# Performance work log

Measured on AMD Instinct MI355X. Metric: run time of the kernel, lower is better.

Reference implementation:

```python
import jax, jax.numpy as jnp
import numpy as np

L, B, T, D, H = 8, 4, 1024, 1024, 16
DH = D // H
TPB, NB = 16, 64  # tokens_per_block, max_blocks; T == TPB*NB
EPS = 1e-5


def _block_causal_mask():
    idx = jnp.arange(T)
    causal = idx[:, None] >= idx[None, :]
    blk = idx // TPB
    block_diag = blk[:, None] == blk[None, :]
    return causal | block_diag  # [T, T] bool


def _ln(x, g, b):
    mu = jnp.mean(x, axis=-1, keepdims=True)
    var = jnp.mean(jnp.square(x - mu), axis=-1, keepdims=True)
    return (x - mu) * jax.lax.rsqrt(var + EPS) * g + b


def setup_inputs() -> dict:
    key = jax.random.key(0)
    ks = jax.random.split(key, 8)
    s = 0.02
    inp = {
        'sequences': jax.random.normal(ks[0], (B, T, D), jnp.float32),
        'Wq': jax.random.normal(ks[1], (L, D, D), jnp.float32) * s,
        'bq': jnp.zeros((L, D), jnp.float32),
        'Wk': jax.random.normal(ks[2], (L, D, D), jnp.float32) * s,
        'bk': jnp.zeros((L, D), jnp.float32),
        'Wv': jax.random.normal(ks[3], (L, D, D), jnp.float32) * s,
        'bv': jnp.zeros((L, D), jnp.float32),
        'Wp': jax.random.normal(ks[4], (L, D, D), jnp.float32) * s,
        'bp': jnp.zeros((L, D), jnp.float32),
        'ln1_g': jnp.ones((L, D), jnp.float32),
        'ln1_b': jnp.zeros((L, D), jnp.float32),
        'ln2_g': jnp.ones((L, D), jnp.float32),
        'ln2_b': jnp.zeros((L, D), jnp.float32),
        'W1': jax.random.normal(ks[5], (L, D, 4 * D), jnp.float32) * s,
        'b1': jnp.zeros((L, 4 * D), jnp.float32),
        'W2': jax.random.normal(ks[6], (L, 4 * D, D), jnp.float32) * s,
        'b2': jnp.zeros((L, D), jnp.float32),
        'lnf_g': jnp.ones((D,), jnp.float32),
        'lnf_b': jnp.zeros((D,), jnp.float32),
    }
    return inp


def reference(sequences, Wq, bq, Wk, bk, Wv, bv, Wp, bp,
              ln1_g, ln1_b, ln2_g, ln2_b, W1, b1, W2, b2, lnf_g, lnf_b):
    mask = _block_causal_mask()
    scale = 1.0 / np.sqrt(DH)
    x = sequences
    for i in range(L):
        h = _ln(x, ln1_g[i], ln1_b[i])
        q = (h @ Wq[i] + bq[i]).reshape(B, T, H, DH)
        k = (h @ Wk[i] + bk[i]).reshape(B, T, H, DH)
        v = (h @ Wv[i] + bv[i]).reshape(B, T, H, DH)
        att = jnp.einsum('bthd,bshd->bhts', q, k) * scale  # [B,H,T,T]
        att = jnp.where(mask, att, -jnp.inf)
        att = jax.nn.softmax(att, axis=-1)
        y = jnp.einsum('bhts,bshd->bthd', att, v).reshape(B, T, D)
        x = x + (y @ Wp[i] + bp[i])
        h2 = _ln(x, ln2_g[i], ln2_b[i])
        ff = jax.nn.gelu(h2 @ W1[i] + b1[i], approximate=False) @ W2[i] + b2[i]
        x = x + ff
    return _ln(x, lnf_g, lnf_b)
```

## Files before the change

### kernel.cpp

```cpp
#include <hip/hip_runtime.h>
#include <hip/hip_bf16.h>
#include <math.h>

#define B_ 4
#define T_ 1024
#define D_ 1024
#define H_ 16
#define DH_ 64
#define M_ 4096
#define QSTR_ 3072
#define EPS_ 1e-5f

typedef __attribute__((ext_vector_type(4))) float f32x4;
typedef __attribute__((ext_vector_type(8))) short s16x8;

#if __has_builtin(__builtin_amdgcn_exp2f)
#define EXP2F __builtin_amdgcn_exp2f
#else
#define EXP2F exp2f
#endif

__device__ __forceinline__ float gelu_f(float x) {
  return 0.5f * x * (1.0f + erff(x * 0.70710678118654752f));
}
__device__ __forceinline__ float b2f(unsigned short u) {
  union { unsigned int i; float f; } c; c.i = ((unsigned int)u) << 16; return c.f;
}
__device__ __forceinline__ unsigned short f2b(float f) {
  __hip_bfloat16 h = __float2bfloat16(f);
  return *reinterpret_cast<unsigned short*>(&h);
}
__device__ __forceinline__ void g2l16(void* l, const void* g) {
  __builtin_amdgcn_global_load_lds(
      (const __attribute__((address_space(1))) void*)g,
      (__attribute__((address_space(3))) void*)l, 16, 0, 0);
}

template<bool BF16OUT>
__global__ __launch_bounds__(256) void ln_kernel(
    const float* __restrict__ in, void* __restrict__ out,
    const float* __restrict__ g, const float* __restrict__ b) {
  const int row = blockIdx.x;
  const int tid = threadIdx.x;
  const float* rp = in + (size_t)row * D_;
  float4 v = *reinterpret_cast<const float4*>(rp + tid * 4);
  float s = v.x + v.y + v.z + v.w;
  float s2 = v.x * v.x + v.y * v.y + v.z * v.z + v.w * v.w;
#pragma unroll
  for (int off = 1; off < 64; off <<= 1) {
    s += __shfl_xor(s, off);
    s2 += __shfl_xor(s2, off);
  }
  __shared__ float red[2][4];
  const int wid = tid >> 6;
  if ((tid & 63) == 0) { red[0][wid] = s; red[1][wid] = s2; }
  __syncthreads();
  s = red[0][0] + red[0][1] + red[0][2] + red[0][3];
  s2 = red[1][0] + red[1][1] + red[1][2] + red[1][3];
  const float mu = s * (1.0f / D_);
  const float var = s2 * (1.0f / D_) - mu * mu;
  const float rs = rsqrtf(var + EPS_);
  float4 gv = *reinterpret_cast<const float4*>(g + tid * 4);
  float4 bv = *reinterpret_cast<const float4*>(b + tid * 4);
  float o0 = (v.x - mu) * rs * gv.x + bv.x;
  float o1 = (v.y - mu) * rs * gv.y + bv.y;
  float o2 = (v.z - mu) * rs * gv.z + bv.z;
  float o3 = (v.w - mu) * rs * gv.w + bv.w;
  if (BF16OUT) {
    ushort4 pk;
    pk.x = f2b(o0); pk.y = f2b(o1); pk.z = f2b(o2); pk.w = f2b(o3);
    *reinterpret_cast<ushort4*>((unsigned short*)out + (size_t)row * D_ + tid * 4) = pk;
  } else {
    *reinterpret_cast<float4*>((float*)out + (size_t)row * D_ + tid * 4) =
        make_float4(o0, o1, o2, o3);
  }
}

__global__ __launch_bounds__(256) void concat_bias(
    const float* __restrict__ bq, const float* __restrict__ bk,
    const float* __restrict__ bv, float* __restrict__ out) {
  const int i = blockIdx.x * 256 + threadIdx.x;
  const int l = i / QSTR_, c = i % QSTR_;
  const float* src = (c < 1024) ? bq : ((c < 2048) ? bk : bv);
  out[i] = src[l * 1024 + (c & 1023)];
}

__device__ __forceinline__ void transpose_tile(
    const float* __restrict__ src, int sld,
    __hip_bfloat16* __restrict__ dst, int dld, int k0, int n0) {
  __shared__ float tile[32][33];
  const int t = threadIdx.x;
  const int r = t >> 3;
  const int cq = (t & 7) * 4;
  float4 vv = *reinterpret_cast<const float4*>(src + (size_t)(k0 + r) * sld + n0 + cq);
  tile[r][cq + 0] = vv.x; tile[r][cq + 1] = vv.y;
  tile[r][cq + 2] = vv.z; tile[r][cq + 3] = vv.w;
  __syncthreads();
  ushort4 o;
  o.x = f2b(tile[cq + 0][r]); o.y = f2b(tile[cq + 1][r]);
  o.z = f2b(tile[cq + 2][r]); o.w = f2b(tile[cq + 3][r]);
  *reinterpret_cast<ushort4*>((unsigned short*)dst + (size_t)(n0 + r) * dld + k0 + cq) = o;
}

struct TPack { const float* s[4]; __hip_bfloat16* d[4]; };

__global__ __launch_bounds__(256) void transpose4(TPack p) {
  transpose_tile(p.s[blockIdx.z], 1024, p.d[blockIdx.z], 1024,
                 blockIdx.x * 32, blockIdx.y * 32);
}
__global__ __launch_bounds__(256) void transpose1(
    const float* __restrict__ src, int sld,
    __hip_bfloat16* __restrict__ dst, int dld) {
  transpose_tile(src, sld, dst, dld, blockIdx.x * 32, blockIdx.y * 32);
}

template<int MODE, int BN>
__global__ __launch_bounds__(256) void gemm_mfma(
    const __hip_bfloat16* __restrict__ A,
    const __hip_bfloat16* __restrict__ Bt,
    const float* __restrict__ bias,
    void* __restrict__ Cout, int N, int K) {
  __shared__ short As[2][128 * 32];
  __shared__ short Bs[2][BN * 32];
  int bid = blockIdx.y * gridDim.x + blockIdx.x;
  const int nwg = gridDim.x * gridDim.y;
  bid = (bid & 7) * (nwg >> 3) + (bid >> 3);
  const int gn = (bid % gridDim.x) * BN;
  const int gm = (bid / gridDim.x) * 128;

  const int tid = threadIdx.x;
  const int wid = tid >> 6, lane = tid & 63;
  constexpr int MR = (BN == 128) ? 4 : 2;
  const int wm = (BN == 128) ? (wid >> 1) : wid;
  const int wn = (BN == 128) ? (wid & 1) : 0;
  const int fr = lane & 15, kg = lane >> 4;

  const int ldr = lane >> 2;
  const int ldk = (lane & 3) * 8;
  const unsigned short* ap =
      (const unsigned short*)A + (size_t)(gm + wid * 32 + ldr) * K + ldk;
  const unsigned short* bp =
      (const unsigned short*)Bt +
      (size_t)(gn + ((BN == 128) ? wid * 32 : wid * 16) + ldr) * K + ldk;

  {
    g2l16((char*)As[0] + (wid * 2) * 1024, ap);
    g2l16((char*)As[0] + (wid * 2 + 1) * 1024, ap + (size_t)16 * K);
    if (BN == 128) {
      g2l16((char*)Bs[0] + (wid * 2) * 1024, bp);
      g2l16((char*)Bs[0] + (wid * 2 + 1) * 1024, bp + (size_t)16 * K);
    } else {
      g2l16((char*)Bs[0] + wid * 1024, bp);
    }
    ap += 32; bp += 32;
  }
  asm volatile("s_waitcnt vmcnt(0)" ::: "memory");
  __syncthreads();

  f32x4 acc[MR][4] = {};
  int cur = 0;
  for (int kt = 0; kt < K; kt += 32) {
    if (kt + 32 < K) {
      g2l16((char*)As[cur ^ 1] + (wid * 2) * 1024, ap);
      g2l16((char*)As[cur ^ 1] + (wid * 2 + 1) * 1024, ap + (size_t)16 * K);
      if (BN == 128) {
        g2l16((char*)Bs[cur ^ 1] + (wid * 2) * 1024, bp);
        g2l16((char*)Bs[cur ^ 1] + (wid * 2 + 1) * 1024, bp + (size_t)16 * K);
      } else {
        g2l16((char*)Bs[cur ^ 1] + wid * 1024, bp);
      }
      ap += 32; bp += 32;
    }
    s16x8 af[MR], bfr[4];
#pragma unroll
    for (int m = 0; m < MR; ++m)
      af[m] = *reinterpret_cast<const s16x8*>(
          &As[cur][(wm * (16 * MR) + m * 16 + fr) * 32 + kg * 8]);
#pragma unroll
    for (int n = 0; n < 4; ++n)
      bfr[n] = *reinterpret_cast<const s16x8*>(
          &Bs[cur][(wn * 64 + n * 16 + fr) * 32 + kg * 8]);
#pragma unroll
    for (int m = 0; m < MR; ++m)
#pragma unroll
      for (int n = 0; n < 4; ++n)
        acc[m][n] = __builtin_amdgcn_mfma_f32_16x16x32_bf16(af[m], bfr[n], acc[m][n], 0, 0, 0);
    asm volatile("s_waitcnt vmcnt(0)" ::: "memory");
    __syncthreads();
    cur ^= 1;
  }

  const int r0 = gm + wm * (16 * MR);
  const int c0 = gn + wn * 64;
  float bb[4];
#pragma unroll
  for (int n = 0; n < 4; ++n)
    bb[n] = bias ? bias[c0 + n * 16 + fr] : 0.0f;
#pragma unroll
  for (int m = 0; m < MR; ++m) {
#pragma unroll
    for (int j = 0; j < 4; ++j) {
      const int row = r0 + m * 16 + kg * 4 + j;
#pragma unroll
      for (int n = 0; n < 4; ++n) {
        float val = acc[m][n][j] + bb[n];
        const size_t idx = (size_t)row * N + c0 + n * 16 + fr;
        if (MODE == 0) {
          ((unsigned short*)Cout)[idx] = f2b(val);
        } else if (MODE == 1) {
          float* cp = (float*)Cout + idx;
          *cp = *cp + val;
        } else {
          ((unsigned short*)Cout)[idx] = f2b(gelu_f(val));
        }
      }
    }
  }
}

__global__ __launch_bounds__(256) void attn_mfma(
    const __hip_bfloat16* __restrict__ qkv, __hip_bfloat16* __restrict__ yg) {
  const int qb = 15 - blockIdx.x;
  const int hh = blockIdx.y;
  const int bb = blockIdx.z;
  __shared__ short Ks[64 * 64];
  __shared__ short Vt[64 * 64];
  __shared__ short Ps[64 * 64];
  const int tid = threadIdx.x;
  const int wid = tid >> 6, lane = tid & 63;
  const int fr = lane & 15, kgv = lane >> 4;
  const size_t qb_base = (size_t)bb * T_ * QSTR_ + (size_t)hh * DH_;
  const unsigned short* qgp = (const unsigned short*)qkv + qb_base;
  const unsigned short* kgp = (const unsigned short*)qkv + qb_base + 1024;
  const unsigned short* vgp = (const unsigned short*)qkv + qb_base + 2048;
  const float C = 0.125f * 1.4426950408889634f;

  {
    const int r8 = lane >> 3, cp = lane & 7;
#pragma unroll
    for (int u = 0; u < 2; ++u) {
      const int row = wid * 16 + u * 8 + r8;
      const int c16 = cp ^ (row & 7);
      g2l16((char*)Ps + (wid * 16 + u * 8) * 128,
            qgp + (size_t)(qb * 64 + row) * QSTR_ + c16 * 8);
    }
  }
  asm volatile("s_waitcnt vmcnt(0)" ::: "memory");
  __syncthreads();
  s16x8 qf[2];
  {
    const int row = wid * 16 + fr;
    const char* rp = (const char*)Ps + row * 128;
    qf[0] = *reinterpret_cast<const s16x8*>(rp + (((0 + kgv) ^ (row & 7)) << 4));
    qf[1] = *reinterpret_cast<const s16x8*>(rp + (((4 + kgv) ^ (row & 7)) << 4));
  }

  f32x4 acco[4] = {};
  float m_run[4] = {-INFINITY, -INFINITY, -INFINITY, -INFINITY};
  float l_run[4] = {};

  for (int kb = 0; kb <= qb; ++kb) {
    __syncthreads();
    {
      const int r8 = lane >> 3, cp = lane & 7;
#pragma unroll
      for (int u = 0; u < 2; ++u) {
        const int row = wid * 16 + u * 8 + r8;
        const int c16 = cp ^ (row & 7);
        g2l16((char*)Ks + (wid * 16 + u * 8) * 128,
              kgp + (size_t)(kb * 64 + row) * QSTR_ + c16 * 8);
      }
    }
    {
      const int kv0 = tid >> 3;
      const int d0 = (tid & 7) * 8;
      const int rot = tid & 7;
#pragma unroll
      for (int u = 0; u < 2; ++u) {
        const int kv = u * 32 + kv0;
        s16x8 sv = *reinterpret_cast<const s16x8*>(
            vgp + (size_t)(kb * 64 + kv) * QSTR_ + d0);
#pragma unroll
        for (int j = 0; j < 8; ++j) {
          const int jj = (j + rot) & 7;
          const int d = d0 + jj;
          *(short*)((char*)Vt + d * 128 + ((((kv >> 3) ^ jj) & 7) << 4) + (kv & 7) * 2) = sv[jj];
        }
      }
    }
    asm volatile("s_waitcnt vmcnt(0)" ::: "memory");
    __syncthreads();

    f32x4 accs[4] = {};
#pragma unroll
    for (int n = 0; n < 4; ++n) {
      const int row = n * 16 + fr;
      const char* rp = (const char*)Ks + row * 128;
      s16x8 kf0 = *reinterpret_cast<const s16x8*>(rp + (((0 + kgv) ^ (row & 7)) << 4));
      s16x8 kf1 = *reinterpret_cast<const s16x8*>(rp + (((4 + kgv) ^ (row & 7)) << 4));
      accs[n] = __builtin_amdgcn_mfma_f32_16x16x32_bf16(qf[0], kf0, accs[n], 0, 0, 0);
      accs[n] = __builtin_amdgcn_mfma_f32_16x16x32_bf16(qf[1], kf1, accs[n], 0, 0, 0);
    }

    const bool diag = (kb == qb);
    float mloc[4];
#pragma unroll
    for (int j = 0; j < 4; ++j) {
      float mm = -3.0e38f;
#pragma unroll
      for (int n = 0; n < 4; ++n)
        if (!(diag && n > wid)) mm = fmaxf(mm, accs[n][j]);
      mloc[j] = mm;
    }
#pragma unroll
    for (int off = 1; off < 16; off <<= 1)
#pragma unroll
      for (int j = 0; j < 4; ++j) mloc[j] = fmaxf(mloc[j], __shfl_xor(mloc[j], off));
    float aj[4];
#pragma unroll
    for (int j = 0; j < 4; ++j) {
      const float mn = fmaxf(m_run[j], mloc[j]);
      aj[j] = EXP2F((m_run[j] - mn) * C);
      m_run[j] = mn;
    }
    float psum[4] = {};
    unsigned short pb[4][4];
#pragma unroll
    for (int n = 0; n < 4; ++n) {
      const bool dead = diag && (n > wid);
#pragma unroll
      for (int j = 0; j < 4; ++j) {
        float p = dead ? 0.0f : EXP2F((accs[n][j] - m_run[j]) * C);
        psum[j] += p;
        pb[n][j] = f2b(p);
      }
    }
#pragma unroll
    for (int j = 0; j < 4; ++j) l_run[j] = l_run[j] * aj[j] + psum[j];
#pragma unroll
    for (int dt = 0; dt < 4; ++dt)
#pragma unroll
      for (int j = 0; j < 4; ++j) acco[dt][j] *= aj[j];
#pragma unroll
    for (int n = 0; n < 4; ++n) {
      const int c16b = n * 2 + (fr >> 3);
#pragma unroll
      for (int j = 0; j < 4; ++j) {
        const int row = wid * 16 + kgv * 4 + j;
        *(short*)((char*)Ps + row * 128 + (((c16b ^ (row & 7)) & 7) << 4) + (fr & 7) * 2) =
            (short)pb[n][j];
      }
    }
#pragma unroll
    for (int kk = 0; kk < 2; ++kk) {
      const int prow = wid * 16 + fr;
      s16x8 pf = *reinterpret_cast<const s16x8*>(
          (const char*)Ps + prow * 128 + ((((kk * 4 + kgv) ^ (prow & 7)) & 7) << 4));
#pragma unroll
      for (int dt = 0; dt < 4; ++dt) {
        const int vrow = dt * 16 + fr;
        s16x8 vf = *reinterpret_cast<const s16x8*>(
            (const char*)Vt + vrow * 128 + ((((kk * 4 + kgv) ^ (vrow & 7)) & 7) << 4));
        acco[dt] = __builtin_amdgcn_mfma_f32_16x16x32_bf16(pf, vf, acco[dt], 0, 0, 0);
      }
    }
  }

#pragma unroll
  for (int off = 1; off < 16; off <<= 1)
#pragma unroll
    for (int j = 0; j < 4; ++j) l_run[j] += __shfl_xor(l_run[j], off);
  float inv[4];
#pragma unroll
  for (int j = 0; j < 4; ++j) inv[j] = 1.0f / l_run[j];
  unsigned short* yp = (unsigned short*)yg + (size_t)bb * T_ * D_ + (size_t)hh * DH_;
#pragma unroll
  for (int dt = 0; dt < 4; ++dt)
#pragma unroll
    for (int j = 0; j < 4; ++j) {
      const int row = qb * 64 + wid * 16 + kgv * 4 + j;
      yp[(size_t)row * D_ + dt * 16 + fr] = f2b(acco[dt][j] * inv[j]);
    }
}

extern "C" void kernel_launch(void* const* d_in, const int* in_sizes, int n_in,
                              void* d_out, int out_size, void* d_ws, size_t ws_size,
                              hipStream_t stream) {
  (void)in_sizes; (void)n_in; (void)out_size; (void)ws_size;
  const float* seq  = (const float*)d_in[0];
  const float* Wq   = (const float*)d_in[1];
  const float* bq   = (const float*)d_in[2];
  const float* Wk   = (const float*)d_in[3];
  const float* bk   = (const float*)d_in[4];
  const float* Wv   = (const float*)d_in[5];
  const float* bv   = (const float*)d_in[6];
  const float* Wp   = (const float*)d_in[7];
  const float* bp   = (const float*)d_in[8];
  const float* ln1g = (const float*)d_in[9];
  const float* ln1b = (const float*)d_in[10];
  const float* ln2g = (const float*)d_in[11];
  const float* ln2b = (const float*)d_in[12];
  const float* W1   = (const float*)d_in[13];
  const float* b1   = (const float*)d_in[14];
  const float* W2   = (const float*)d_in[15];
  const float* b2   = (const float*)d_in[16];
  const float* lnfg = (const float*)d_in[17];
  const float* lnfb = (const float*)d_in[18];

  float* x = (float*)d_out;
  char* ws = (char*)d_ws;
  const size_t MB = 1024ull * 1024ull;
  typedef __hip_bfloat16 bf16;
  bf16*  wtqkv = (bf16*)(ws + 0 * MB);
  bf16*  wtp   = (bf16*)(ws + 6 * MB);
  bf16*  wtF1  = (bf16*)(ws + 8 * MB);
  bf16*  wtF2  = (bf16*)(ws + 16 * MB);
  bf16*  hb    = (bf16*)(ws + 24 * MB);
  bf16*  qkv   = (bf16*)(ws + 32 * MB);
  bf16*  mid   = (bf16*)(ws + 56 * MB);
  float* bqkv  = (float*)(ws + 88 * MB);

  hipMemcpyAsync(x, seq, (size_t)M_ * D_ * sizeof(float), hipMemcpyDeviceToDevice, stream);

  const dim3 blk(256);
  concat_bias<<<96, blk, 0, stream>>>(bq, bk, bv, bqkv);

  for (int i = 0; i < 8; ++i) {
    const size_t wo  = (size_t)i * D_ * D_;
    const size_t vo  = (size_t)i * D_;
    const size_t w1o = (size_t)i * D_ * 4 * D_;

    ln_kernel<true><<<M_, blk, 0, stream>>>(x, hb, ln1g + vo, ln1b + vo);
    TPack tp;
    tp.s[0] = Wq + wo; tp.s[1] = Wk + wo; tp.s[2] = Wv + wo; tp.s[3] = Wp + wo;
    tp.d[0] = wtqkv; tp.d[1] = wtqkv + 1024 * 1024; tp.d[2] = wtqkv + 2048 * 1024;
    tp.d[3] = wtp;
    transpose4<<<dim3(32, 32, 4), blk, 0, stream>>>(tp);
    gemm_mfma<0, 128><<<dim3(24, 32), blk, 0, stream>>>(
        hb, wtqkv, bqkv + (size_t)i * QSTR_, qkv, QSTR_, 1024);
    attn_mfma<<<dim3(16, 16, 4), blk, 0, stream>>>(qkv, hb);
    gemm_mfma<1, 64><<<dim3(16, 32), blk, 0, stream>>>(hb, wtp, bp + vo, x, 1024, 1024);
    ln_kernel<true><<<M_, blk, 0, stream>>>(x, hb, ln2g + vo, ln2b + vo);
    transpose1<<<dim3(32, 128), blk, 0, stream>>>(W1 + w1o, 4096, wtF1, 1024);
    gemm_mfma<2, 128><<<dim3(32, 32), blk, 0, stream>>>(
        hb, wtF1, b1 + (size_t)i * 4096, mid, 4096, 1024);
    transpose1<<<dim3(128, 32), blk, 0, stream>>>(W2 + w1o, 1024, wtF2, 4096);
    gemm_mfma<1, 64><<<dim3(16, 32), blk, 0, stream>>>(
        mid, wtF2, b2 + vo, x, 1024, 4096);
  }
  ln_kernel<false><<<M_, blk, 0, stream>>>(x, x, lnfg, lnfb);
}
```

Measured before the change: 2.441 ms.

## Process 128 query rows per attention block and fuse all weight transposes

```diff
diff --git a/kernel.cpp b/kernel.cpp
--- a/kernel.cpp
+++ b/kernel.cpp
@@ -102,16 +102,32 @@
   *reinterpret_cast<ushort4*>((unsigned short*)dst + (size_t)(n0 + r) * dld + k0 + cq) = o;
 }
 
-struct TPack { const float* s[4]; __hip_bfloat16* d[4]; };
-
-__global__ __launch_bounds__(256) void transpose4(TPack p) {
-  transpose_tile(p.s[blockIdx.z], 1024, p.d[blockIdx.z], 1024,
-                 blockIdx.x * 32, blockIdx.y * 32);
-}
-__global__ __launch_bounds__(256) void transpose1(
-    const float* __restrict__ src, int sld,
-    __hip_bfloat16* __restrict__ dst, int dld) {
-  transpose_tile(src, sld, dst, dld, blockIdx.x * 32, blockIdx.y * 32);
+struct TrAll {
+  const float *wq, *wk, *wv, *wp, *w1, *w2;
+  __hip_bfloat16 *dqkv, *dp, *d1, *d2;
+};
+
+__global__ __launch_bounds__(256) void transpose_all(TrAll a) {
+  const int t = blockIdx.x;
+  const float* src;
+  __hip_bfloat16* dst;
+  int sld, dld, k0, n0;
+  if (t < 4096) {
+    const int m = t >> 10, tile = t & 1023;
+    k0 = (tile >> 5) * 32; n0 = (tile & 31) * 32;
+    src = (m == 0) ? a.wq : (m == 1) ? a.wk : (m == 2) ? a.wv : a.wp;
+    sld = 1024; dld = 1024;
+    dst = (m < 3) ? (a.dqkv + (size_t)m * 1024 * 1024) : a.dp;
+  } else if (t < 8192) {
+    const int tile = t - 4096;
+    k0 = (tile & 31) * 32; n0 = (tile >> 5) * 32;
+    src = a.w1; sld = 4096; dst = a.d1; dld = 1024;
+  } else {
+    const int tile = t - 8192;
+    k0 = (tile >> 5) * 32; n0 = (tile & 31) * 32;
+    src = a.w2; sld = 1024; dst = a.d2; dld = 4096;
+  }
+  transpose_tile(src, sld, dst, dld, k0, n0);
 }
 
 template<int MODE, int BN>
@@ -220,46 +236,52 @@
 
 __global__ __launch_bounds__(256) void attn_mfma(
     const __hip_bfloat16* __restrict__ qkv, __hip_bfloat16* __restrict__ yg) {
-  const int qb = 15 - blockIdx.x;
+  const int qb = 7 - blockIdx.x;
   const int hh = blockIdx.y;
   const int bb = blockIdx.z;
+  __shared__ short Qs[128 * 64];
   __shared__ short Ks[64 * 64];
   __shared__ short Vt[64 * 64];
-  __shared__ short Ps[64 * 64];
   const int tid = threadIdx.x;
   const int wid = tid >> 6, lane = tid & 63;
-  const int fr = lane & 15, kgv = lane >> 4;
+  const int fr = lane & 15, kg = lane >> 4;
   const size_t qb_base = (size_t)bb * T_ * QSTR_ + (size_t)hh * DH_;
   const unsigned short* qgp = (const unsigned short*)qkv + qb_base;
-  const unsigned short* kgp = (const unsigned short*)qkv + qb_base + 1024;
-  const unsigned short* vgp = (const unsigned short*)qkv + qb_base + 2048;
+  const unsigned short* kgp = qgp + 1024;
+  const unsigned short* vgp = qgp + 2048;
   const float C = 0.125f * 1.4426950408889634f;
 
   {
     const int r8 = lane >> 3, cp = lane & 7;
 #pragma unroll
-    for (int u = 0; u < 2; ++u) {
-      const int row = wid * 16 + u * 8 + r8;
+    for (int u = 0; u < 4; ++u) {
+      const int row = wid * 32 + u * 8 + r8;
       const int c16 = cp ^ (row & 7);
-      g2l16((char*)Ps + (wid * 16 + u * 8) * 128,
-            qgp + (size_t)(qb * 64 + row) * QSTR_ + c16 * 8);
+      g2l16((char*)Qs + (wid * 32 + u * 8) * 128,
+            qgp + (size_t)(qb * 128 + row) * QSTR_ + c16 * 8);
     }
   }
   asm volatile("s_waitcnt vmcnt(0)" ::: "memory");
   __syncthreads();
-  s16x8 qf[2];
-  {
-    const int row = wid * 16 + fr;
-    const char* rp = (const char*)Ps + row * 128;
-    qf[0] = *reinterpret_cast<const s16x8*>(rp + (((0 + kgv) ^ (row & 7)) << 4));
-    qf[1] = *reinterpret_cast<const s16x8*>(rp + (((4 + kgv) ^ (row & 7)) << 4));
-  }
-
-  f32x4 acco[4] = {};
-  float m_run[4] = {-INFINITY, -INFINITY, -INFINITY, -INFINITY};
-  float l_run[4] = {};
-
-  for (int kb = 0; kb <= qb; ++kb) {
+  s16x8 qf[2][2];
+#pragma unroll
+  for (int rg = 0; rg < 2; ++rg) {
+    const int row = wid * 32 + rg * 16 + fr;
+    const char* rp = (const char*)Qs + row * 128;
+    qf[rg][0] = *reinterpret_cast<const s16x8*>(rp + (((0 + kg) ^ (row & 7)) << 4));
+    qf[rg][1] = *reinterpret_cast<const s16x8*>(rp + (((4 + kg) ^ (row & 7)) << 4));
+  }
+
+  f32x4 acco[2][4] = {};
+  float m_run[2][4], l_run[2][4];
+#pragma unroll
+  for (int rg = 0; rg < 2; ++rg)
+#pragma unroll
+    for (int j = 0; j < 4; ++j) { m_run[rg][j] = -INFINITY; l_run[rg][j] = 0.f; }
+
+  const int q16hi = qb * 8 + wid * 2 + 1;
+  const int ntile = 2 * qb + 2;
+  for (int kt = 0; kt < ntile; ++kt) {
     __syncthreads();
     {
       const int r8 = lane >> 3, cp = lane & 7;
@@ -268,7 +290,7 @@
         const int row = wid * 16 + u * 8 + r8;
         const int c16 = cp ^ (row & 7);
         g2l16((char*)Ks + (wid * 16 + u * 8) * 128,
-              kgp + (size_t)(kb * 64 + row) * QSTR_ + c16 * 8);
+              kgp + (size_t)(kt * 64 + row) * QSTR_ + c16 * 8);
       }
     }
     {
@@ -279,7 +301,7 @@
       for (int u = 0; u < 2; ++u) {
         const int kv = u * 32 + kv0;
         s16x8 sv = *reinterpret_cast<const s16x8*>(
-            vgp + (size_t)(kb * 64 + kv) * QSTR_ + d0);
+            vgp + (size_t)(kt * 64 + kv) * QSTR_ + d0);
 #pragma unroll
         for (int j = 0; j < 8; ++j) {
           const int jj = (j + rot) & 7;
@@ -291,96 +313,101 @@
     asm volatile("s_waitcnt vmcnt(0)" ::: "memory");
     __syncthreads();
 
-    f32x4 accs[4] = {};
-#pragma unroll
-    for (int n = 0; n < 4; ++n) {
-      const int row = n * 16 + fr;
-      const char* rp = (const char*)Ks + row * 128;
-      s16x8 kf0 = *reinterpret_cast<const s16x8*>(rp + (((0 + kgv) ^ (row & 7)) << 4));
-      s16x8 kf1 = *reinterpret_cast<const s16x8*>(rp + (((4 + kgv) ^ (row & 7)) << 4));
-      accs[n] = __builtin_amdgcn_mfma_f32_16x16x32_bf16(qf[0], kf0, accs[n], 0, 0, 0);
-      accs[n] = __builtin_amdgcn_mfma_f32_16x16x32_bf16(qf[1], kf1, accs[n], 0, 0, 0);
-    }
-
-    const bool diag = (kb == qb);
-    float mloc[4];
-#pragma unroll
-    for (int j = 0; j < 4; ++j) {
-      float mm = -3.0e38f;
-#pragma unroll
-      for (int n = 0; n < 4; ++n)
-        if (!(diag && n > wid)) mm = fmaxf(mm, accs[n][j]);
-      mloc[j] = mm;
-    }
-#pragma unroll
-    for (int off = 1; off < 16; off <<= 1)
-#pragma unroll
-      for (int j = 0; j < 4; ++j) mloc[j] = fmaxf(mloc[j], __shfl_xor(mloc[j], off));
-    float aj[4];
-#pragma unroll
-    for (int j = 0; j < 4; ++j) {
-      const float mn = fmaxf(m_run[j], mloc[j]);
-      aj[j] = EXP2F((m_run[j] - mn) * C);
-      m_run[j] = mn;
-    }
-    float psum[4] = {};
-    unsigned short pb[4][4];
-#pragma unroll
-    for (int n = 0; n < 4; ++n) {
-      const bool dead = diag && (n > wid);
+    if (kt * 4 <= q16hi) {
+      f32x4 accs[2][4] = {};
+#pragma unroll
+      for (int n = 0; n < 4; ++n) {
+        const int row = n * 16 + fr;
+        const char* rp = (const char*)Ks + row * 128;
+        s16x8 kf0 = *reinterpret_cast<const s16x8*>(rp + (((0 + kg) ^ (row & 7)) << 4));
+        s16x8 kf1 = *reinterpret_cast<const s16x8*>(rp + (((4 + kg) ^ (row & 7)) << 4));
+#pragma unroll
+        for (int rg = 0; rg < 2; ++rg) {
+          accs[rg][n] = __builtin_amdgcn_mfma_f32_16x16x32_bf16(qf[rg][0], kf0, accs[rg][n], 0, 0, 0);
+          accs[rg][n] = __builtin_amdgcn_mfma_f32_16x16x32_bf16(qf[rg][1], kf1, accs[rg][n], 0, 0, 0);
+        }
+      }
+#pragma unroll
+      for (int rg = 0; rg < 2; ++rg) {
+        const int q16 = qb * 8 + wid * 2 + rg;
+        float mloc[4] = {-3.0e38f, -3.0e38f, -3.0e38f, -3.0e38f};
+#pragma unroll
+        for (int n = 0; n < 4; ++n)
+          if (kt * 4 + n <= q16)
+#pragma unroll
+            for (int j = 0; j < 4; ++j) mloc[j] = fmaxf(mloc[j], accs[rg][n][j]);
+#pragma unroll
+        for (int off = 1; off < 16; off <<= 1)
+#pragma unroll
+          for (int j = 0; j < 4; ++j) mloc[j] = fmaxf(mloc[j], __shfl_xor(mloc[j], off));
+        float a_[4];
+#pragma unroll
+        for (int j = 0; j < 4; ++j) {
+          const float mn = fmaxf(m_run[rg][j], mloc[j]);
+          a_[j] = EXP2F((m_run[rg][j] - mn) * C);
+          m_run[rg][j] = mn;
+        }
+        float psum[4] = {};
+#pragma unroll
+        for (int n = 0; n < 4; ++n) {
+          const bool dead = (kt * 4 + n > q16);
+          const int c16b = n * 2 + (fr >> 3);
+#pragma unroll
+          for (int j = 0; j < 4; ++j) {
+            float p = dead ? 0.0f : EXP2F((accs[rg][n][j] - m_run[rg][j]) * C);
+            psum[j] += p;
+            const int row = wid * 32 + rg * 16 + kg * 4 + j;
+            *(short*)((char*)Qs + row * 128 + (((c16b ^ (row & 7)) & 7) << 4) + (fr & 7) * 2) =
+                (short)f2b(p);
+          }
+        }
+#pragma unroll
+        for (int j = 0; j < 4; ++j) l_run[rg][j] = l_run[rg][j] * a_[j] + psum[j];
+#pragma unroll
+        for (int dt = 0; dt < 4; ++dt)
+#pragma unroll
+          for (int j = 0; j < 4; ++j) acco[rg][dt][j] *= a_[j];
+      }
+#pragma unroll
+      for (int rg = 0; rg < 2; ++rg) {
+        const int prow = wid * 32 + rg * 16 + fr;
+        const char* pp = (const char*)Qs + prow * 128;
+#pragma unroll
+        for (int kk = 0; kk < 2; ++kk) {
+          const s16x8 pf = *reinterpret_cast<const s16x8*>(
+              pp + ((((kk * 4 + kg) ^ (prow & 7)) & 7) << 4));
+#pragma unroll
+          for (int dt = 0; dt < 4; ++dt) {
+            const int vrow = dt * 16 + fr;
+            const s16x8 vf = *reinterpret_cast<const s16x8*>(
+                (const char*)Vt + vrow * 128 + ((((kk * 4 + kg) ^ (vrow & 7)) & 7) << 4));
+            acco[rg][dt] = __builtin_amdgcn_mfma_f32_16x16x32_bf16(pf, vf, acco[rg][dt], 0, 0, 0);
+          }
+        }
+      }
+    }
+  }
+
+#pragma unroll
+  for (int off = 1; off < 16; off <<= 1)
+#pragma unroll
+    for (int rg = 0; rg < 2; ++rg)
+#pragma unroll
+      for (int j = 0; j < 4; ++j) l_run[rg][j] += __shfl_xor(l_run[rg][j], off);
+  unsigned short* yp = (unsigned short*)yg + (size_t)bb * T_ * D_ + (size_t)hh * DH_;
+#pragma unroll
+  for (int rg = 0; rg < 2; ++rg) {
+    float inv[4];
+#pragma unroll
+    for (int j = 0; j < 4; ++j) inv[j] = 1.0f / l_run[rg][j];
+#pragma unroll
+    for (int dt = 0; dt < 4; ++dt)
 #pragma unroll
       for (int j = 0; j < 4; ++j) {
-        float p = dead ? 0.0f : EXP2F((accs[n][j] - m_run[j]) * C);
-        psum[j] += p;
-        pb[n][j] = f2b(p);
-      }
-    }
-#pragma unroll
-    for (int j = 0; j < 4; ++j) l_run[j] = l_run[j] * aj[j] + psum[j];
-#pragma unroll
-    for (int dt = 0; dt < 4; ++dt)
-#pragma unroll
-      for (int j = 0; j < 4; ++j) acco[dt][j] *= aj[j];
-#pragma unroll
-    for (int n = 0; n < 4; ++n) {
-      const int c16b = n * 2 + (fr >> 3);
-#pragma unroll
-      for (int j = 0; j < 4; ++j) {
-        const int row = wid * 16 + kgv * 4 + j;
-        *(short*)((char*)Ps + row * 128 + (((c16b ^ (row & 7)) & 7) << 4) + (fr & 7) * 2) =
-            (short)pb[n][j];
-      }
-    }
-#pragma unroll
-    for (int kk = 0; kk < 2; ++kk) {
-      const int prow = wid * 16 + fr;
-      s16x8 pf = *reinterpret_cast<const s16x8*>(
-          (const char*)Ps + prow * 128 + ((((kk * 4 + kgv) ^ (prow & 7)) & 7) << 4));
-#pragma unroll
-      for (int dt = 0; dt < 4; ++dt) {
-        const int vrow = dt * 16 + fr;
-        s16x8 vf = *reinterpret_cast<const s16x8*>(
-            (const char*)Vt + vrow * 128 + ((((kk * 4 + kgv) ^ (vrow & 7)) & 7) << 4));
-        acco[dt] = __builtin_amdgcn_mfma_f32_16x16x32_bf16(pf, vf, acco[dt], 0, 0, 0);
-      }
-    }
-  }
-
-#pragma unroll
-  for (int off = 1; off < 16; off <<= 1)
-#pragma unroll
-    for (int j = 0; j < 4; ++j) l_run[j] += __shfl_xor(l_run[j], off);
-  float inv[4];
-#pragma unroll
-  for (int j = 0; j < 4; ++j) inv[j] = 1.0f / l_run[j];
-  unsigned short* yp = (unsigned short*)yg + (size_t)bb * T_ * D_ + (size_t)hh * DH_;
-#pragma unroll
-  for (int dt = 0; dt < 4; ++dt)
-#pragma unroll
-    for (int j = 0; j < 4; ++j) {
-      const int row = qb * 64 + wid * 16 + kgv * 4 + j;
-      yp[(size_t)row * D_ + dt * 16 + fr] = f2b(acco[dt][j] * inv[j]);
-    }
+        const int row = qb * 128 + wid * 32 + rg * 16 + kg * 4 + j;
+        yp[(size_t)row * D_ + dt * 16 + fr] = f2b(acco[rg][dt][j] * inv[j]);
+      }
+  }
 }
 
 extern "C" void kernel_launch(void* const* d_in, const int* in_sizes, int n_in,
@@ -431,20 +458,18 @@
     const size_t w1o = (size_t)i * D_ * 4 * D_;
 
     ln_kernel<true><<<M_, blk, 0, stream>>>(x, hb, ln1g + vo, ln1b + vo);
-    TPack tp;
-    tp.s[0] = Wq + wo; tp.s[1] = Wk + wo; tp.s[2] = Wv + wo; tp.s[3] = Wp + wo;
-    tp.d[0] = wtqkv; tp.d[1] = wtqkv + 1024 * 1024; tp.d[2] = wtqkv + 2048 * 1024;
-    tp.d[3] = wtp;
-    transpose4<<<dim3(32, 32, 4), blk, 0, stream>>>(tp);
+    TrAll ta;
+    ta.wq = Wq + wo; ta.wk = Wk + wo; ta.wv = Wv + wo; ta.wp = Wp + wo;
+    ta.w1 = W1 + w1o; ta.w2 = W2 + w1o;
+    ta.dqkv = wtqkv; ta.dp = wtp; ta.d1 = wtF1; ta.d2 = wtF2;
+    transpose_all<<<12288, blk, 0, stream>>>(ta);
     gemm_mfma<0, 128><<<dim3(24, 32), blk, 0, stream>>>(
         hb, wtqkv, bqkv + (size_t)i * QSTR_, qkv, QSTR_, 1024);
-    attn_mfma<<<dim3(16, 16, 4), blk, 0, stream>>>(qkv, hb);
+    attn_mfma<<<dim3(8, 16, 4), blk, 0, stream>>>(qkv, hb);
     gemm_mfma<1, 64><<<dim3(16, 32), blk, 0, stream>>>(hb, wtp, bp + vo, x, 1024, 1024);
     ln_kernel<true><<<M_, blk, 0, stream>>>(x, hb, ln2g + vo, ln2b + vo);
-    transpose1<<<dim3(32, 128), blk, 0, stream>>>(W1 + w1o, 4096, wtF1, 1024);
     gemm_mfma<2, 128><<<dim3(32, 32), blk, 0, stream>>>(
         hb, wtF1, b1 + (size_t)i * 4096, mid, 4096, 1024);
-    transpose1<<<dim3(128, 32), blk, 0, stream>>>(W2 + w1o, 1024, wtF2, 4096);
     gemm_mfma<1, 64><<<dim3(16, 32), blk, 0, stream>>>(
         mid, wtF2, b2 + vo, x, 1024, 4096);
   }
```

After: 2.305 ms. 1.06x faster.
